# Performance work log

Hardware: AMD Instinct MI355X
Metric: run time of the kernel (lower is better)

Reference implementation:

```python
import jax, jax.numpy as jnp
import numpy as np

N = 768  # length of time vector

def setup_inputs() -> dict:
    key = jax.random.key(0)
    ks = jax.random.split(key, 4)
    # time vector (sorted grid-like values, as in a GP time axis)
    x = jnp.sort(jax.random.uniform(ks[0], (N,), dtype=jnp.float32) * (6 * np.pi))
    # MLP params: Linear(2,1024) -> Sigmoid -> Linear(1024,128) -> ReLU -> Linear(128,1)
    W1 = jax.random.normal(ks[1], (1024, 2), dtype=jnp.float32) * (1.0 / np.sqrt(2.0))
    b1 = jnp.zeros((1024,), dtype=jnp.float32)
    W2 = jax.random.normal(ks[2], (128, 1024), dtype=jnp.float32) * (1.0 / np.sqrt(1024.0))
    b2 = jnp.zeros((128,), dtype=jnp.float32)
    W3 = jax.random.normal(ks[3], (1, 128), dtype=jnp.float32) * (1.0 / np.sqrt(128.0))
    b3 = jnp.zeros((1,), dtype=jnp.float32)
    return {"x": x, "W1": W1, "b1": b1, "W2": W2, "b2": b2, "W3": W3, "b3": b3}


def reference(x, W1, b1, W2, b2, W3, b3):
    n = x.shape[0]
    # all (i, j) with j >= i  -> n(n+1)/2 pairs; replaces the Python double loop
    iu, ju = jnp.triu_indices(n)
    pairs = jnp.stack([x[iu], x[ju]], axis=-1)            # [P, 2]
    h = jax.nn.sigmoid(pairs @ W1.T + b1)                 # [P, 1024]
    h = jax.nn.relu(h @ W2.T + b2)                        # [P, 128]
    v = (h @ W3.T + b3)[:, 0]                             # [P]
    # K starts as eye; upper triangle INCLUDING diagonal is overwritten
    K = jnp.eye(n, dtype=x.dtype).at[iu, ju].set(v)       # [n, n] upper-triangular
    return K.T @ K                                        # symmetric PSD covariance
```

## Files before the change

### kernel.cpp

```cpp
#include <hip/hip_runtime.h>
#include <hip/hip_bf16.h>

#define NN 768
#define MD 1024
#define NPAIR 295296
#define NPBLK2 2307

typedef __attribute__((ext_vector_type(8))) short s16x8;
typedef __attribute__((ext_vector_type(4))) float f32x4;
typedef __attribute__((ext_vector_type(2))) float f32x2;
typedef __attribute__((ext_vector_type(2))) __bf16 b16x2;

__device__ __forceinline__ ushort bf16_rn(float f) {
    uint u = __builtin_bit_cast(uint, f);
    u += 0x7FFFu + ((u >> 16) & 1u);
    return (ushort)(u >> 16);
}

__device__ __forceinline__ void ptoij(int p, int& io, int& jo) {
    const float disc = (float)(1537 * 1537 - 8 * p);
    int i = (int)((1537.0f - sqrtf(disc)) * 0.5f);
    i = i < 0 ? 0 : (i > 767 ? 767 : i);
    while (i > 0 && p < i * (1537 - i) / 2) --i;
    while (i < 767 && p >= (i + 1) * (1536 - i) / 2) ++i;
    io = i;
    jo = i + (p - i * (1537 - i) / 2);
}

#define GLOAD16(gsrc, ldst)                                                        \
    __builtin_amdgcn_global_load_lds(                                              \
        (const __attribute__((address_space(1))) void*)(gsrc),                     \
        (__attribute__((address_space(3))) void*)(ldst), 16, 0, 0)

__global__ __launch_bounds__(256) void w2bf16(const float* __restrict__ W2,
                                              ushort* __restrict__ WhiS)
{
    const int id = blockIdx.x * 256 + threadIdx.x;
    const int k = id >> 7;
    const int m = (id & 127) * 8;
    const float4 a = *reinterpret_cast<const float4*>(W2 + k * MD + m);
    const float4 b = *reinterpret_cast<const float4*>(W2 + k * MD + m + 4);
    const float w[8] = {a.x, a.y, a.z, a.w, b.x, b.y, b.z, b.w};
    s16x8 h;
#pragma unroll
    for (int e = 0; e < 8; ++e) h[e] = (short)bf16_rn(w[e]);
    const int c = m >> 6;
    const int mloc8 = (m >> 3) & 7;
    const int byte = (mloc8 * 16) ^ ((k & 7) << 4);
    const int off = c * 8192 + ((k * 128 + byte) >> 1);
    *reinterpret_cast<s16x8*>(&WhiS[off]) = h;
}

#define STAGE(cc)                                                            \
    {                                                                        \
        const ushort* sh_ = WhiS + (cc) * 8192;                              \
        ushort* ld_ = Wh[(cc) & 1];                                          \
        _Pragma("unroll")                                                    \
        for (int q_ = 0; q_ < 4; ++q_) {                                     \
            const int off_ = (wv * 4 + q_) * 512;                            \
            GLOAD16(sh_ + off_ + lane * 8, ld_ + off_);                      \
        }                                                                    \
    }

#define SIG_CHUNK(cc, dst)                                                   \
    {                                                                        \
        _Pragma("unroll")                                                    \
        for (int ks_ = 0; ks_ < 2; ++ks_) {                                  \
            const int m0_ = (cc) * 64 + ks_ * 32 + l4 * 8;                   \
            const f32x4 a0_ = *reinterpret_cast<const f32x4*>(&sa[m0_]);     \
            const f32x4 a1_ = *reinterpret_cast<const f32x4*>(&sa[m0_ + 4]); \
            const f32x4 c0_ = *reinterpret_cast<const f32x4*>(&sc[m0_]);     \
            const f32x4 c1_ = *reinterpret_cast<const f32x4*>(&sc[m0_ + 4]); \
            const f32x4 b0_ = *reinterpret_cast<const f32x4*>(&sb[m0_]);     \
            const f32x4 b1_ = *reinterpret_cast<const f32x4*>(&sb[m0_ + 4]); \
            _Pragma("unroll")                                                \
            for (int tm_ = 0; tm_ < 2; ++tm_) {                              \
                const f32x2 xi2_ = (f32x2){xia[tm_], xia[tm_]};              \
                const f32x2 xj2_ = (f32x2){xja[tm_], xja[tm_]};              \
                const f32x2 one2_ = (f32x2){1.f, 1.f};                       \
                union { s16x8 v; uint u[4]; } fr_;                           \
                _Pragma("unroll")                                            \
                for (int h_ = 0; h_ < 4; ++h_) {                             \
                    f32x2 av_, cv_, bv_;                                     \
                    if (h_ < 2) {                                            \
                        av_ = (f32x2){a0_[2 * h_], a0_[2 * h_ + 1]};         \
                        cv_ = (f32x2){c0_[2 * h_], c0_[2 * h_ + 1]};         \
                        bv_ = (f32x2){b0_[2 * h_], b0_[2 * h_ + 1]};         \
                    } else {                                                 \
                        av_ = (f32x2){a1_[2 * h_ - 4], a1_[2 * h_ - 3]};     \
                        cv_ = (f32x2){c1_[2 * h_ - 4], c1_[2 * h_ - 3]};     \
                        bv_ = (f32x2){b1_[2 * h_ - 4], b1_[2 * h_ - 3]};     \
                    }                                                        \
                    const f32x2 u2_ = __builtin_elementwise_fma(             \
                        xi2_, av_, __builtin_elementwise_fma(xj2_, cv_, bv_));\
                    f32x2 e2_;                                               \
                    e2_[0] = __builtin_amdgcn_exp2f(u2_[0]);                 \
                    e2_[1] = __builtin_amdgcn_exp2f(u2_[1]);                 \
                    const f32x2 t2_ = e2_ + one2_;                           \
                    b16x2 p_;                                                \
                    p_.x = (__bf16)__builtin_amdgcn_rcpf(t2_[0]);            \
                    p_.y = (__bf16)__builtin_amdgcn_rcpf(t2_[1]);            \
                    fr_.u[h_] = __builtin_bit_cast(uint, p_);                \
                }                                                            \
                dst[ks_][tm_] = fr_.v;                                       \
            }                                                                \
        }                                                                    \
    }

#define MFMA_STEP(cc, src)                                                   \
    {                                                                        \
        const ushort* wb_ = Wh[(cc) & 1];                                    \
        _Pragma("unroll")                                                    \
        for (int ks_ = 0; ks_ < 2; ++ks_) {                                  \
            _Pragma("unroll")                                                \
            for (int th_ = 0; th_ < 2; ++th_) {                              \
                s16x8 bh_[4];                                                \
                _Pragma("unroll")                                            \
                for (int tn_ = 0; tn_ < 4; ++tn_) {                          \
                    const int k_ = th_ * 64 + tn_ * 16 + l15;                \
                    const int byte_ = (ks_ * 64 + l4 * 16) ^ ((k_ & 7) << 4);\
                    const int idx_ = (k_ * 128 + byte_) >> 1;                \
                    bh_[tn_] = *reinterpret_cast<const s16x8*>(&wb_[idx_]);  \
                }                                                            \
                __builtin_amdgcn_s_setprio(1);                               \
                _Pragma("unroll")                                            \
                for (int tm_ = 0; tm_ < 2; ++tm_)                            \
                    _Pragma("unroll")                                        \
                    for (int tn_ = 0; tn_ < 4; ++tn_)                        \
                        acc[tm_][th_][tn_] = __builtin_amdgcn_mfma_f32_16x16x32_bf16( \
                            src[ks_][tm_], bh_[tn_], acc[tm_][th_][tn_], 0, 0, 0);    \
                __builtin_amdgcn_s_setprio(0);                               \
            }                                                                \
        }                                                                    \
    }

__global__ __launch_bounds__(256, 3) void mlp_pairs(
    const float* __restrict__ x,
    const float* __restrict__ W1, const float* __restrict__ b1,
    const ushort* __restrict__ WhiS,
    const float* __restrict__ b2, const float* __restrict__ W3,
    const float* __restrict__ b3, float* __restrict__ K)
{
    __shared__ __align__(16) float sa[MD], sc[MD], sb[MD];
    __shared__ __align__(16) ushort Wh[2][8192];

    const int t = threadIdx.x;
    const int lane = t & 63, wv = t >> 6;
    const int l15 = lane & 15, l4 = lane >> 4;

    const float NL2E = -1.4426950408889634f;
    for (int m = t; m < MD; m += 256) {
        const float2 w = reinterpret_cast<const float2*>(W1)[m];
        sa[m] = w.x * NL2E;
        sc[m] = w.y * NL2E;
        sb[m] = b1[m] * NL2E;
    }

    const int pairbase = blockIdx.x * 128 + wv * 32;

    float xia[2], xja[2];
#pragma unroll
    for (int tm = 0; tm < 2; ++tm) {
        const int p = pairbase + tm * 16 + l15;
        if (p < NPAIR) {
            int i, j;
            ptoij(p, i, j);
            xia[tm] = x[i];
            xja[tm] = x[j];
        } else {
            xia[tm] = 0.f;
            xja[tm] = 0.f;
        }
    }

    f32x4 acc[2][2][4];
#pragma unroll
    for (int a = 0; a < 2; ++a)
#pragma unroll
        for (int th = 0; th < 2; ++th)
#pragma unroll
            for (int b = 0; b < 4; ++b) acc[a][th][b] = (f32x4){0.f, 0.f, 0.f, 0.f};

    STAGE(0);
    __syncthreads();

    s16x8 ah[2][2];
    for (int c = 0; c < 16; ++c) {
        if (c < 15) STAGE(c + 1);
        SIG_CHUNK(c, ah);
        MFMA_STEP(c, ah);
        __syncthreads();
    }

    float w3v[2][4], b2v[2][4];
#pragma unroll
    for (int th = 0; th < 2; ++th)
#pragma unroll
        for (int tn = 0; tn < 4; ++tn) {
            const int k = th * 64 + tn * 16 + l15;
            w3v[th][tn] = W3[k];
            b2v[th][tn] = b2[k];
        }
    const float b3v = b3[0];
#pragma unroll
    for (int tm = 0; tm < 2; ++tm)
#pragma unroll
        for (int r = 0; r < 4; ++r) {
            float v = 0.f;
#pragma unroll
            for (int th = 0; th < 2; ++th)
#pragma unroll
                for (int tn = 0; tn < 4; ++tn)
                    v = fmaf(w3v[th][tn], fmaxf(acc[tm][th][tn][r] + b2v[th][tn], 0.f), v);
            v += __shfl_xor(v, 1, 16);
            v += __shfl_xor(v, 2, 16);
            v += __shfl_xor(v, 4, 16);
            v += __shfl_xor(v, 8, 16);
            if (l15 == 0) {
                const int p = pairbase + tm * 16 + l4 * 4 + r;
                if (p < NPAIR) {
                    int i, j;
                    ptoij(p, i, j);
                    K[i * NN + j] = v + b3v;
                }
            }
        }
}

#define MC 32
#define JT 128
#define SPAD 132
__global__ __launch_bounds__(256) void mlp_fill(
    const float* __restrict__ x,
    const float* __restrict__ W1, const float* __restrict__ b1,
    const float* __restrict__ W2, const float* __restrict__ b2,
    const float* __restrict__ W3, const float* __restrict__ b3,
    float* __restrict__ K)
{
    const int i  = blockIdx.y;
    const int j0 = blockIdx.x * JT;
    if (j0 + JT - 1 < i) return;
    __shared__ float sA[MD];
    __shared__ float sCw[MD];
    __shared__ float sxj[JT];
    __shared__ float S[MC][SPAD];
    __shared__ float W2t[MC][SPAD];
    const int t = threadIdx.x;
    const float xi = x[i];
    for (int m = t; m < MD; m += 256) {
        const float2 w = reinterpret_cast<const float2*>(W1)[m];
        sA[m]  = fmaf(xi, w.x, b1[m]);
        sCw[m] = w.y;
    }
    if (t < JT) sxj[t] = x[j0 + t];
    const int tk = t & 15;
    const int tj = t >> 4;
    float w3r[8], b2r[8];
#pragma unroll
    for (int kk = 0; kk < 8; kk++) {
        w3r[kk] = W3[tk * 8 + kk];
        b2r[kk] = b2[tk * 8 + kk];
    }
    float acc[8][8];
#pragma unroll
    for (int jj = 0; jj < 8; jj++)
#pragma unroll
        for (int kk = 0; kk < 8; kk++) acc[jj][kk] = 0.f;
    const int jx   = t & 127;
    const int mseg = (t >> 7) * 16;
    __syncthreads();
    const float xjv = sxj[jx];
    for (int m0 = 0; m0 < MD; m0 += MC) {
#pragma unroll
        for (int q = 0; q < 4; q++) {
            const int f   = t + q * 256;
            const int k   = f >> 3;
            const int mm4 = (f & 7) * 4;
            const float4 w = *reinterpret_cast<const float4*>(W2 + k * MD + m0 + mm4);
            W2t[mm4 + 0][k] = w.x;
            W2t[mm4 + 1][k] = w.y;
            W2t[mm4 + 2][k] = w.z;
            W2t[mm4 + 3][k] = w.w;
        }
#pragma unroll
        for (int q = 0; q < 16; q++) {
            const int ml = mseg + q;
            const float z = fmaf(xjv, sCw[m0 + ml], sA[m0 + ml]);
            S[ml][jx] = 1.0f / (1.0f + __expf(-z));
        }
        __syncthreads();
#pragma unroll 4
        for (int mm = 0; mm < MC; mm++) {
            const float4 s0 = *reinterpret_cast<const float4*>(&S[mm][tj * 8]);
            const float4 s1 = *reinterpret_cast<const float4*>(&S[mm][tj * 8 + 4]);
            const float4 w0 = *reinterpret_cast<const float4*>(&W2t[mm][tk * 8]);
            const float4 w1 = *reinterpret_cast<const float4*>(&W2t[mm][tk * 8 + 4]);
            const float sj[8] = {s0.x, s0.y, s0.z, s0.w, s1.x, s1.y, s1.z, s1.w};
            const float wk[8] = {w0.x, w0.y, w0.z, w0.w, w1.x, w1.y, w1.z, w1.w};
#pragma unroll
            for (int jj = 0; jj < 8; jj++)
#pragma unroll
                for (int kk = 0; kk < 8; kk++)
                    acc[jj][kk] = fmaf(sj[jj], wk[kk], acc[jj][kk]);
        }
        __syncthreads();
    }
    const float b3v = b3[0];
#pragma unroll
    for (int jj = 0; jj < 8; jj++) {
        float v = 0.f;
#pragma unroll
        for (int kk = 0; kk < 8; kk++) {
            const float h = acc[jj][kk] + b2r[kk];
            v = fmaf(w3r[kk], fmaxf(h, 0.f), v);
        }
#pragma unroll
        for (int off = 8; off >= 1; off >>= 1)
            v += __shfl_xor(v, off, 16);
        if (tk == 0) {
            const int j = j0 + tj * 8 + jj;
            if (j >= i) K[i * NN + j] = v + b3v;
        }
    }
}

__global__ __launch_bounds__(256) void ktk(const float* __restrict__ K,
                                           float* __restrict__ C)
{
    const int b0 = blockIdx.x * 64;
    const int a0 = blockIdx.y * 64;
    if (b0 < a0) return;
    __shared__ float Ka[64][68];
    __shared__ float Kb[64][68];
    const int t  = threadIdx.x;
    const int tb = t & 15;
    const int ta = t >> 4;
    float acc[4][4];
#pragma unroll
    for (int u = 0; u < 4; u++)
#pragma unroll
        for (int v = 0; v < 4; v++) acc[u][v] = 0.f;
    const int kmax = a0 + 64;
    for (int k0 = 0; k0 < kmax; k0 += 64) {
#pragma unroll
        for (int q = 0; q < 4; q++) {
            const int f  = t + q * 256;
            const int kk = f >> 4;
            const int c4 = (f & 15) * 4;
            *reinterpret_cast<float4*>(&Ka[kk][c4]) =
                *reinterpret_cast<const float4*>(K + (k0 + kk) * NN + a0 + c4);
            *reinterpret_cast<float4*>(&Kb[kk][c4]) =
                *reinterpret_cast<const float4*>(K + (k0 + kk) * NN + b0 + c4);
        }
        __syncthreads();
#pragma unroll 8
        for (int kk = 0; kk < 64; kk++) {
            const float4 av = *reinterpret_cast<const float4*>(&Ka[kk][ta * 4]);
            const float4 bv = *reinterpret_cast<const float4*>(&Kb[kk][tb * 4]);
            const float a4[4] = {av.x, av.y, av.z, av.w};
            const float b4[4] = {bv.x, bv.y, bv.z, bv.w};
#pragma unroll
            for (int u = 0; u < 4; u++)
#pragma unroll
                for (int v = 0; v < 4; v++)
                    acc[u][v] = fmaf(a4[u], b4[v], acc[u][v]);
        }
        __syncthreads();
    }
#pragma unroll
    for (int u = 0; u < 4; u++) {
        float4 o;
        o.x = acc[u][0]; o.y = acc[u][1]; o.z = acc[u][2]; o.w = acc[u][3];
        *reinterpret_cast<float4*>(C + (a0 + ta * 4 + u) * NN + b0 + tb * 4) = o;
    }
    if (b0 > a0) {
#pragma unroll
        for (int v = 0; v < 4; v++) {
            float4 o;
            o.x = acc[0][v]; o.y = acc[1][v]; o.z = acc[2][v]; o.w = acc[3][v];
            *reinterpret_cast<float4*>(C + (b0 + tb * 4 + v) * NN + a0 + ta * 4) = o;
        }
    }
}

extern "C" void kernel_launch(void* const* d_in, const int* in_sizes, int n_in,
                              void* d_out, int out_size, void* d_ws, size_t ws_size,
                              hipStream_t stream)
{
    const float* x  = (const float*)d_in[0];
    const float* W1 = (const float*)d_in[1];
    const float* b1 = (const float*)d_in[2];
    const float* W2 = (const float*)d_in[3];
    const float* b2 = (const float*)d_in[4];
    const float* W3 = (const float*)d_in[5];
    const float* b3 = (const float*)d_in[6];
    float* Kmat = (float*)d_ws;
    float* C    = (float*)d_out;

    const size_t kBytes = (size_t)NN * NN * sizeof(float);
    const size_t need   = kBytes + 262144;

    hipMemsetAsync(Kmat, 0, kBytes, stream);
    if (ws_size >= need) {
        ushort* WhiS = (ushort*)((char*)d_ws + kBytes);
        w2bf16<<<64, 256, 0, stream>>>(W2, WhiS);
        mlp_pairs<<<NPBLK2, 256, 0, stream>>>(x, W1, b1, WhiS, b2, W3, b3, Kmat);
    } else {
        mlp_fill<<<dim3(6, NN), 256, 0, stream>>>(x, W1, b1, W2, b2, W3, b3, Kmat);
    }
    ktk<<<dim3(NN / 64, NN / 64), 256, 0, stream>>>(Kmat, C);
}
```

Before: 174.4 us.

## Load W2 MFMA fragments directly into registers instead of staging through LDS

The W2 preprocessing kernel now writes bf16 weights in the exact per-lane MFMA B-fragment order, so the main kernel can load B operands straight from global memory (L2-resident) into registers. This removes the LDS double buffer, the async global-to-LDS staging and the per-chunk __syncthreads, and prefetches the next half-chunk's fragments while the current MFMAs run. The cost is more VGPR pressure (8 B fragments plus 16 accumulators) and reliance on L2/L1 bandwidth for repeated weight reads across all blocks.

```diff
diff --git a/kernel.cpp b/kernel.cpp
--- a/kernel.cpp
+++ b/kernel.cpp
@@ -27,39 +27,32 @@
     jo = i + (p - i * (1537 - i) / 2);
 }
 
-#define GLOAD16(gsrc, ldst)                                                        \
-    __builtin_amdgcn_global_load_lds(                                              \
-        (const __attribute__((address_space(1))) void*)(gsrc),                     \
-        (__attribute__((address_space(3))) void*)(ldst), 16, 0, 0)
-
-__global__ __launch_bounds__(256) void w2bf16(const float* __restrict__ W2,
-                                              ushort* __restrict__ WhiS)
+__global__ __launch_bounds__(256) void w2frag(const float* __restrict__ W2,
+                                              ushort* __restrict__ WF)
 {
     const int id = blockIdx.x * 256 + threadIdx.x;
-    const int k = id >> 7;
-    const int m = (id & 127) * 8;
+    const int lane = id & 63;
+    const int f = id >> 6;
+    const int tn = f & 7;
+    const int ks = (f >> 3) & 1;
+    const int c  = f >> 4;
+    const int k = tn * 16 + (lane & 15);
+    const int m = c * 64 + ks * 32 + (lane >> 4) * 8;
     const float4 a = *reinterpret_cast<const float4*>(W2 + k * MD + m);
     const float4 b = *reinterpret_cast<const float4*>(W2 + k * MD + m + 4);
     const float w[8] = {a.x, a.y, a.z, a.w, b.x, b.y, b.z, b.w};
     s16x8 h;
 #pragma unroll
     for (int e = 0; e < 8; ++e) h[e] = (short)bf16_rn(w[e]);
-    const int c = m >> 6;
-    const int mloc8 = (m >> 3) & 7;
-    const int byte = (mloc8 * 16) ^ ((k & 7) << 4);
-    const int off = c * 8192 + ((k * 128 + byte) >> 1);
-    *reinterpret_cast<s16x8*>(&WhiS[off]) = h;
-}
-
-#define STAGE(cc)                                                            \
+    *reinterpret_cast<s16x8*>(WF + id * 8) = h;
+}
+
+#define LOADB(cc, ks)                                                        \
     {                                                                        \
-        const ushort* sh_ = WhiS + (cc) * 8192;                              \
-        ushort* ld_ = Wh[(cc) & 1];                                          \
+        const ushort* wb_ = WF + (cc) * 8192 + (ks) * 4096 + lane * 8;       \
         _Pragma("unroll")                                                    \
-        for (int q_ = 0; q_ < 4; ++q_) {                                     \
-            const int off_ = (wv * 4 + q_) * 512;                            \
-            GLOAD16(sh_ + off_ + lane * 8, ld_ + off_);                      \
-        }                                                                    \
+        for (int tn_ = 0; tn_ < 8; ++tn_)                                    \
+            bh[tn_] = *reinterpret_cast<const s16x8*>(wb_ + tn_ * 512);      \
     }
 
 #define SIG_CHUNK(cc, dst)                                                   \
@@ -107,46 +100,31 @@
         }                                                                    \
     }
 
-#define MFMA_STEP(cc, src)                                                   \
+#define MFMA_HALF(ks)                                                        \
     {                                                                        \
-        const ushort* wb_ = Wh[(cc) & 1];                                    \
+        __builtin_amdgcn_s_setprio(1);                                       \
         _Pragma("unroll")                                                    \
-        for (int ks_ = 0; ks_ < 2; ++ks_) {                                  \
+        for (int tm_ = 0; tm_ < 2; ++tm_)                                    \
             _Pragma("unroll")                                                \
-            for (int th_ = 0; th_ < 2; ++th_) {                              \
-                s16x8 bh_[4];                                                \
-                _Pragma("unroll")                                            \
-                for (int tn_ = 0; tn_ < 4; ++tn_) {                          \
-                    const int k_ = th_ * 64 + tn_ * 16 + l15;                \
-                    const int byte_ = (ks_ * 64 + l4 * 16) ^ ((k_ & 7) << 4);\
-                    const int idx_ = (k_ * 128 + byte_) >> 1;                \
-                    bh_[tn_] = *reinterpret_cast<const s16x8*>(&wb_[idx_]);  \
-                }                                                            \
-                __builtin_amdgcn_s_setprio(1);                               \
-                _Pragma("unroll")                                            \
-                for (int tm_ = 0; tm_ < 2; ++tm_)                            \
-                    _Pragma("unroll")                                        \
-                    for (int tn_ = 0; tn_ < 4; ++tn_)                        \
-                        acc[tm_][th_][tn_] = __builtin_amdgcn_mfma_f32_16x16x32_bf16( \
-                            src[ks_][tm_], bh_[tn_], acc[tm_][th_][tn_], 0, 0, 0);    \
-                __builtin_amdgcn_s_setprio(0);                               \
-            }                                                                \
-        }                                                                    \
-    }
-
-__global__ __launch_bounds__(256, 3) void mlp_pairs(
+            for (int tn_ = 0; tn_ < 8; ++tn_)                                \
+                acc[tm_][tn_] = __builtin_amdgcn_mfma_f32_16x16x32_bf16(     \
+                    ah[ks][tm_], bh[tn_], acc[tm_][tn_], 0, 0, 0);           \
+        __builtin_amdgcn_s_setprio(0);                                       \
+    }
+
+__global__ __launch_bounds__(256, 3) void mlp_pairs_reg(
     const float* __restrict__ x,
     const float* __restrict__ W1, const float* __restrict__ b1,
-    const ushort* __restrict__ WhiS,
+    const ushort* __restrict__ WF,
     const float* __restrict__ b2, const float* __restrict__ W3,
     const float* __restrict__ b3, float* __restrict__ K)
 {
     __shared__ __align__(16) float sa[MD], sc[MD], sb[MD];
-    __shared__ __align__(16) ushort Wh[2][8192];
 
     const int t = threadIdx.x;
-    const int lane = t & 63, wv = t >> 6;
+    const int lane = t & 63;
     const int l15 = lane & 15, l4 = lane >> 4;
+    const int wv = t >> 6;
 
     const float NL2E = -1.4426950408889634f;
     for (int m = t; m < MD; m += 256) {
@@ -173,34 +151,32 @@
         }
     }
 
-    f32x4 acc[2][2][4];
+    f32x4 acc[2][8];
 #pragma unroll
     for (int a = 0; a < 2; ++a)
 #pragma unroll
-        for (int th = 0; th < 2; ++th)
-#pragma unroll
-            for (int b = 0; b < 4; ++b) acc[a][th][b] = (f32x4){0.f, 0.f, 0.f, 0.f};
-
-    STAGE(0);
+        for (int b = 0; b < 8; ++b) acc[a][b] = (f32x4){0.f, 0.f, 0.f, 0.f};
+
+    s16x8 bh[8];
+    LOADB(0, 0);
     __syncthreads();
 
     s16x8 ah[2][2];
     for (int c = 0; c < 16; ++c) {
-        if (c < 15) STAGE(c + 1);
         SIG_CHUNK(c, ah);
-        MFMA_STEP(c, ah);
-        __syncthreads();
-    }
-
-    float w3v[2][4], b2v[2][4];
-#pragma unroll
-    for (int th = 0; th < 2; ++th)
-#pragma unroll
-        for (int tn = 0; tn < 4; ++tn) {
-            const int k = th * 64 + tn * 16 + l15;
-            w3v[th][tn] = W3[k];
-            b2v[th][tn] = b2[k];
-        }
+        MFMA_HALF(0);
+        LOADB(c, 1);
+        MFMA_HALF(1);
+        if (c < 15) LOADB(c + 1, 0);
+    }
+
+    float w3v[8], b2v[8];
+#pragma unroll
+    for (int tn = 0; tn < 8; ++tn) {
+        const int k = tn * 16 + l15;
+        w3v[tn] = W3[k];
+        b2v[tn] = b2[k];
+    }
     const float b3v = b3[0];
 #pragma unroll
     for (int tm = 0; tm < 2; ++tm)
@@ -208,10 +184,8 @@
         for (int r = 0; r < 4; ++r) {
             float v = 0.f;
 #pragma unroll
-            for (int th = 0; th < 2; ++th)
-#pragma unroll
-                for (int tn = 0; tn < 4; ++tn)
-                    v = fmaf(w3v[th][tn], fmaxf(acc[tm][th][tn][r] + b2v[th][tn], 0.f), v);
+            for (int tn = 0; tn < 8; ++tn)
+                v = fmaf(w3v[tn], fmaxf(acc[tm][tn][r] + b2v[tn], 0.f), v);
             v += __shfl_xor(v, 1, 16);
             v += __shfl_xor(v, 2, 16);
             v += __shfl_xor(v, 4, 16);
@@ -402,9 +376,9 @@
 
     hipMemsetAsync(Kmat, 0, kBytes, stream);
     if (ws_size >= need) {
-        ushort* WhiS = (ushort*)((char*)d_ws + kBytes);
-        w2bf16<<<64, 256, 0, stream>>>(W2, WhiS);
-        mlp_pairs<<<NPBLK2, 256, 0, stream>>>(x, W1, b1, WhiS, b2, W3, b3, Kmat);
+        ushort* WF = (ushort*)((char*)d_ws + kBytes);
+        w2frag<<<64, 256, 0, stream>>>(W2, WF);
+        mlp_pairs_reg<<<NPBLK2, 256, 0, stream>>>(x, W1, b1, WF, b2, W3, b3, Kmat);
     } else {
         mlp_fill<<<dim3(6, NN), 256, 0, stream>>>(x, W1, b1, W2, b2, W3, b3, Kmat);
     }
```

Measured after the change: 169.0 us. 1.03x faster.
